# Kernel tuning notes

Hardware: AMD Instinct MI355X
Metric: run time of the kernel (lower is better)

The kernel has to match this reference:

```python
import jax, jax.numpy as jnp
import numpy as np

B, T = 1, 1024
HIDDEN = 5376
N_HEADS = 32
N_KV = 4
HEAD_DIM = 512          # global_head_dim (full-attention layer)
ROT_DIM = 128           # head_dim * full_partial_rotary_factor (0.25)
MAX_SEQ = 4096
THETA = 1000000.0       # full_rope_theta
EPS = 1e-6


def _precompute_freqs(rot_dim, max_seq, theta, freq_base_dim):
    # freq exponent uses full head_dim (freq_base_dim) for partial rotary
    freqs = 1.0 / (theta ** (np.arange(0, rot_dim, 2, dtype=np.float32) / freq_base_dim))
    t = np.arange(max_seq, dtype=np.float32)
    ang = np.outer(t, freqs)                      # [max_seq, rot_dim//2]
    return jnp.asarray(np.cos(ang)), jnp.asarray(np.sin(ang))


def setup_inputs() -> dict:
    key = jax.random.key(0)
    ks = jax.random.split(key, 6)
    x = jax.random.normal(ks[0], (B, T, HIDDEN), jnp.float32)
    wq = jax.random.normal(ks[1], (HIDDEN, N_HEADS * HEAD_DIM), jnp.float32) * 0.02
    wk = jax.random.normal(ks[2], (HIDDEN, N_KV * HEAD_DIM), jnp.float32) * 0.02
    wo = jax.random.normal(ks[3], (N_HEADS * HEAD_DIM, HIDDEN), jnp.float32) * 0.02
    q_norm_w = 1.0 + 0.01 * jax.random.normal(ks[4], (HEAD_DIM,), jnp.float32)
    k_norm_w = 1.0 + 0.01 * jax.random.normal(ks[5], (HEAD_DIM,), jnp.float32)
    input_pos = jnp.arange(T, dtype=jnp.int32)    # prefill positions 0..T-1
    # causal mask over the full cache length: key slot s visible iff s <= query pos
    attn_mask = (jnp.arange(MAX_SEQ)[None, :] <= input_pos[:, None])[None, None]  # [1,1,T,S] bool
    fc, fs = _precompute_freqs(ROT_DIM, MAX_SEQ, THETA, HEAD_DIM)
    k_cache = jnp.zeros((B, N_KV, MAX_SEQ, HEAD_DIM), jnp.float32)
    v_cache = jnp.zeros_like(k_cache)
    return dict(x=x, input_pos=input_pos, attn_mask=attn_mask, wq=wq, wk=wk, wo=wo,
                q_norm_w=q_norm_w, k_norm_w=k_norm_w, k_cache=k_cache, v_cache=v_cache,
                freqs_cos=fc, freqs_sin=fs)


def _rmsnorm(x, w=None):
    y = x * jax.lax.rsqrt(jnp.mean(x * x, axis=-1, keepdims=True) + EPS)
    return y * w if w is not None else y


def _rope(t, cos, sin):
    # t: (B,H,T,D); rotate only the first ROT_DIM dims (interleaved pairs), pass the rest
    rot, pas = t[..., :ROT_DIM], t[..., ROT_DIM:]
    r = rot.reshape(rot.shape[:-1] + (ROT_DIM // 2, 2))
    tr, ti = r[..., 0], r[..., 1]
    c = cos[None, None]  # (1,1,T,ROT_DIM//2)
    s = sin[None, None]
    out = jnp.stack([tr * c - ti * s, tr * s + ti * c], axis=-1).reshape(rot.shape)
    return jnp.concatenate([out, pas], axis=-1)


def reference(x, input_pos, attn_mask, wq, wk, wo, q_norm_w, k_norm_w,
              k_cache, v_cache, freqs_cos, freqs_sin):
    q = (x @ wq).reshape(B, T, N_HEADS, HEAD_DIM)
    raw_k = (x @ wk).reshape(B, T, N_KV, HEAD_DIM)   # k_eq_v: raw_v = raw_k
    q = _rmsnorm(q, q_norm_w)
    k = _rmsnorm(raw_k, k_norm_w)
    v = _rmsnorm(raw_k)                               # RMSNormNoWeight on shared K=V
    q = q.transpose(0, 2, 1, 3)                       # (B,H,T,D)
    k = k.transpose(0, 2, 1, 3)
    v = v.transpose(0, 2, 1, 3)
    cos = freqs_cos[input_pos]
    sin = freqs_sin[input_pos]
    q = _rope(q, cos, sin)
    k = _rope(k, cos, sin)
    # KV cache update (index_copy along seq dim)
    k_cache = k_cache.at[:, :, input_pos, :].set(k)
    v_cache = v_cache.at[:, :, input_pos, :].set(v)
    # GQA SDPA with scale=1.0, grouped to avoid materializing repeated K/V
    G = N_HEADS // N_KV
    qg = q.reshape(B, N_KV, G, T, HEAD_DIM)
    scores = jnp.einsum('bkgtd,bksd->bkgts', qg, k_cache)
    neg = jnp.finfo(scores.dtype).min
    scores = jnp.where(attn_mask[:, :, None], scores, neg)  # (1,1,1,T,S) broadcast
    attn = jax.nn.softmax(scores, axis=-1)
    y = jnp.einsum('bkgts,bksd->bkgtd', attn, v_cache).reshape(B, N_HEADS, T, HEAD_DIM)
    y = y.transpose(0, 2, 1, 3).reshape(B, T, N_HEADS * HEAD_DIM)
    return y @ wo
```

## Files before the change

kernel.cpp:

```cpp
#include <hip/hip_runtime.h>
#include <stdint.h>

typedef unsigned short u16;
typedef _Float16 f16;
typedef f16 f16x8 __attribute__((ext_vector_type(8)));
typedef float f32x4 __attribute__((ext_vector_type(4)));
typedef unsigned short u16x4 __attribute__((ext_vector_type(4)));
typedef unsigned short u16x8 __attribute__((ext_vector_type(8)));

#define MFMA16(a, b, c) __builtin_amdgcn_mfma_f32_16x16x32_f16(a, b, c, 0, 0, 0)

__device__ __forceinline__ u16 f2h_u(float f) {
  union { f16 h; u16 u; } v; v.h = (f16)f; return v.u;
}
__device__ __forceinline__ float h2f(u16 u) {
  union { u16 u; f16 h; } v; v.u = u; return (float)v.h;
}
__device__ __forceinline__ f16x8 ld_h8(const u16* p) {
  return *(const f16x8*)p;
}
__device__ __forceinline__ void gl_lds16(const u16* g, u16* l) {
  __builtin_amdgcn_global_load_lds(
      (const __attribute__((address_space(1))) void*)g,
      (__attribute__((address_space(3))) void*)l, 16, 0, 0);
}

__global__ __launch_bounds__(256) void convert_f32_f16(
    const float* __restrict__ in, u16* __restrict__ out, int n8)
{
  int i = blockIdx.x * 256 + threadIdx.x;
  int stride = gridDim.x * 256;
  for (; i < n8; i += stride) {
    f32x4 a = *(const f32x4*)(in + (size_t)i * 8);
    f32x4 b = *(const f32x4*)(in + (size_t)i * 8 + 4);
    u16x8 o;
#pragma unroll
    for (int j = 0; j < 4; ++j) { o[j] = f2h_u(a[j]); o[4 + j] = f2h_u(b[j]); }
    *(u16x8*)(out + (size_t)i * 8) = o;
  }
}

__global__ __launch_bounds__(256) void transpose_f32_f16(
    const float* __restrict__ in, u16* __restrict__ out,
    int R, int C, int ldi, int ldo)
{
  __shared__ u16 tile[64 * 66];
  int x0 = blockIdx.x * 64, y0 = blockIdx.y * 64;
  int t = threadIdx.x;
  int xr = (t & 15) * 4;
  int yr = t >> 4;
#pragma unroll
  for (int p = 0; p < 4; ++p) {
    int y = yr + p * 16;
    f32x4 v = *(const f32x4*)(in + (size_t)(y0 + y) * ldi + x0 + xr);
    tile[y * 66 + xr + 0] = f2h_u(v[0]);
    tile[y * 66 + xr + 1] = f2h_u(v[1]);
    tile[y * 66 + xr + 2] = f2h_u(v[2]);
    tile[y * 66 + xr + 3] = f2h_u(v[3]);
  }
  __syncthreads();
#pragma unroll
  for (int p = 0; p < 4; ++p) {
    int x = (t >> 4) + p * 16;
    int yq = (t & 15) * 4;
    u16x4 v;
    v.x = tile[(yq + 0) * 66 + x];
    v.y = tile[(yq + 1) * 66 + x];
    v.z = tile[(yq + 2) * 66 + x];
    v.w = tile[(yq + 3) * 66 + x];
    *(u16x4*)(out + (size_t)(x0 + x) * ldo + y0 + yq) = v;
  }
}

__global__ __launch_bounds__(256) void transpose_h16(
    const u16* __restrict__ in, u16* __restrict__ out,
    int R, int C, int ldi, int ldo, long zin, long zout)
{
  __shared__ u16 tile[64 * 66];
  const u16* ip = in + (size_t)blockIdx.z * zin;
  u16* op = out + (size_t)blockIdx.z * zout;
  int x0 = blockIdx.x * 64, y0 = blockIdx.y * 64;
  int t = threadIdx.x;
  int xr = (t & 15) * 4;
  int yr = t >> 4;
#pragma unroll
  for (int p = 0; p < 4; ++p) {
    int y = yr + p * 16;
    u16x4 v = *(const u16x4*)(ip + (size_t)(y0 + y) * ldi + x0 + xr);
    tile[y * 66 + xr + 0] = v.x;
    tile[y * 66 + xr + 1] = v.y;
    tile[y * 66 + xr + 2] = v.z;
    tile[y * 66 + xr + 3] = v.w;
  }
  __syncthreads();
#pragma unroll
  for (int p = 0; p < 4; ++p) {
    int x = (t >> 4) + p * 16;
    int yq = (t & 15) * 4;
    u16x4 v;
    v.x = tile[(yq + 0) * 66 + x];
    v.y = tile[(yq + 1) * 66 + x];
    v.z = tile[(yq + 2) * 66 + x];
    v.w = tile[(yq + 3) * 66 + x];
    *(u16x4*)(op + (size_t)(x0 + x) * ldo + y0 + yq) = v;
  }
}

template <bool F32OUT>
__global__ __launch_bounds__(512, 4) void gemm_bt(
    const u16* __restrict__ A, const u16* __restrict__ Bt, void* __restrict__ Cv,
    int Ksp, int lda, int ldb, int ldc, long zstride)
{
  __shared__ alignas(16) u16 As[3 * 256 * 32];
  __shared__ alignas(16) u16 Bs[3 * 128 * 32];
  int tid = threadIdx.x;
  int lane = tid & 63;
  int wave = tid >> 6;
  int wm = wave >> 2, wn = wave & 3;
  int r15 = lane & 15, g = lane >> 4;

  int gx = gridDim.x, gy = gridDim.y;
  int nwg = gx * gy;
  int flat = blockIdx.y * gx + blockIdx.x;
  int q = nwg >> 3, rr = nwg & 7, xcd = flat & 7, lo = flat >> 3;
  int s = ((xcd < rr) ? xcd * (q + 1) : rr * (q + 1) + (xcd - rr) * q) + lo;
  int by = s % gy;
  int bx = s / gy;
  int row0 = by * 256, col0 = bx * 128;
  int kbeg = blockIdx.z * Ksp;

  int rA = tid >> 2;
  int pc = tid & 3;
  int cs = pc ^ ((rA >> 1) & 3);
  const u16* Ag0 = A  + (size_t)(row0 + rA) * lda + kbeg + cs * 8;
  const u16* Ag1 = Ag0 + (size_t)128 * lda;
  const u16* Bg  = Bt + (size_t)(col0 + rA) * ldb + kbeg + cs * 8;

  f32x4 acc[8][2];
#pragma unroll
  for (int i = 0; i < 8; ++i)
#pragma unroll
    for (int j = 0; j < 2; ++j) acc[i][j] = (f32x4){0.f, 0.f, 0.f, 0.f};

  int nk = Ksp >> 5;

  auto STAGE = [&](int kk, int b) {
    u16* la = As + b * 8192 + wave * 512;
    u16* lb = Bs + b * 4096 + wave * 512;
    gl_lds16(Ag0 + (size_t)kk * 32, la);
    gl_lds16(Ag1 + (size_t)kk * 32, la + 4096);
    gl_lds16(Bg  + (size_t)kk * 32, lb);
  };

  STAGE(0, 0);
  STAGE(1, 1);
  asm volatile("s_waitcnt vmcnt(3)" ::: "memory");
  __builtin_amdgcn_s_barrier();

  int swz = (g ^ ((r15 >> 1) & 3)) * 8;
  int b0 = 0;
  for (int k = 0; k < nk; ++k) {
    const u16* Ab = As + b0 * 8192;
    const u16* Bb = Bs + b0 * 4096;
    f16x8 bfr[2], af[4];
#pragma unroll
    for (int ni = 0; ni < 2; ++ni)
      bfr[ni] = ld_h8(Bb + (wn * 32 + ni * 16 + r15) * 32 + swz);
#pragma unroll
    for (int m2 = 0; m2 < 4; ++m2)
      af[m2] = ld_h8(Ab + (wm * 128 + m2 * 16 + r15) * 32 + swz);
    if (k + 2 < nk) {
      int b2 = b0 + 2; if (b2 >= 3) b2 -= 3;
      STAGE(k + 2, b2);
    }
    __builtin_amdgcn_s_setprio(1);
#pragma unroll
    for (int m2 = 0; m2 < 4; ++m2)
#pragma unroll
      for (int ni = 0; ni < 2; ++ni)
        acc[m2][ni] = MFMA16(af[m2], bfr[ni], acc[m2][ni]);
    f16x8 ag[4];
#pragma unroll
    for (int m2 = 0; m2 < 4; ++m2)
      ag[m2] = ld_h8(Ab + (wm * 128 + (4 + m2) * 16 + r15) * 32 + swz);
#pragma unroll
    for (int m2 = 0; m2 < 4; ++m2)
#pragma unroll
      for (int ni = 0; ni < 2; ++ni)
        acc[4 + m2][ni] = MFMA16(ag[m2], bfr[ni], acc[4 + m2][ni]);
    __builtin_amdgcn_s_setprio(0);
    if (k <= nk - 3) {
      asm volatile("s_waitcnt vmcnt(3)" ::: "memory");
    } else {
      asm volatile("s_waitcnt vmcnt(0)" ::: "memory");
    }
    asm volatile("s_waitcnt lgkmcnt(0)" ::: "memory");
    __builtin_amdgcn_s_barrier();
    b0 = (b0 == 2) ? 0 : b0 + 1;
  }

#pragma unroll
  for (int mi = 0; mi < 8; ++mi)
#pragma unroll
    for (int ni = 0; ni < 2; ++ni) {
      int row = row0 + wm * 128 + mi * 16 + g * 4;
      int col = col0 + wn * 32 + ni * 16 + r15;
#pragma unroll
      for (int r = 0; r < 4; ++r) {
        if constexpr (F32OUT)
          ((float*)Cv)[(size_t)blockIdx.z * zstride + (size_t)(row + r) * ldc + col] = acc[mi][ni][r];
        else
          ((u16*)Cv)[(size_t)(row + r) * ldc + col] = f2h_u(acc[mi][ni][r]);
      }
    }
}

__global__ __launch_bounds__(256) void reduce_add2_f32(
    const float* __restrict__ p, float* __restrict__ out, int n4, long half)
{
  int i = blockIdx.x * 256 + threadIdx.x;
  int stride = gridDim.x * 256;
  for (; i < n4; i += stride) {
    f32x4 a = *(const f32x4*)(p + (size_t)i * 4);
    f32x4 b = *(const f32x4*)(p + half + (size_t)i * 4);
    *(f32x4*)(out + (size_t)i * 4) = a + b;
  }
}

__global__ __launch_bounds__(256) void reduce_add4_f16(
    const float* __restrict__ p, u16* __restrict__ out, int n4, long zs)
{
  int i = blockIdx.x * 256 + threadIdx.x;
  int stride = gridDim.x * 256;
  for (; i < n4; i += stride) {
    f32x4 a = *(const f32x4*)(p + (size_t)i * 4);
    a += *(const f32x4*)(p + zs + (size_t)i * 4);
    a += *(const f32x4*)(p + 2 * zs + (size_t)i * 4);
    a += *(const f32x4*)(p + 3 * zs + (size_t)i * 4);
    u16x4 o;
#pragma unroll
    for (int j = 0; j < 4; ++j) o[j] = f2h_u(a[j]);
    *(u16x4*)(out + (size_t)i * 4) = o;
  }
}

__global__ __launch_bounds__(64) void norm_rope_q(
    u16* __restrict__ q, const float* __restrict__ w,
    const float* __restrict__ fc, const float* __restrict__ fs)
{
  int t = blockIdx.x, h = blockIdx.y, lane = threadIdx.x;
  u16* row = q + (size_t)t * 16384 + h * 512;
  u16x8 v = *(const u16x8*)(row + lane * 8);
  float x[8];
  float ss = 0.f;
#pragma unroll
  for (int j = 0; j < 8; ++j) { x[j] = h2f(v[j]); ss += x[j] * x[j]; }
#pragma unroll
  for (int m = 1; m < 64; m <<= 1) ss += __shfl_xor(ss, m, 64);
  float rms = rsqrtf(ss * (1.f / 512.f) + 1e-6f);
  f32x4 w0 = *(const f32x4*)(w + lane * 8);
  f32x4 w1 = *(const f32x4*)(w + lane * 8 + 4);
  float y[8];
#pragma unroll
  for (int j = 0; j < 4; ++j) {
    y[j] = x[j] * rms * w0[j];
    y[4 + j] = x[4 + j] * rms * w1[j];
  }
  if (lane < 16) {
    f32x4 cv = *(const f32x4*)(fc + t * 64 + lane * 4);
    f32x4 sv = *(const f32x4*)(fs + t * 64 + lane * 4);
#pragma unroll
    for (int j = 0; j < 4; ++j) {
      float c = cv[j], s = sv[j];
      float a = y[2 * j], b = y[2 * j + 1];
      y[2 * j] = a * c - b * s;
      y[2 * j + 1] = a * s + b * c;
    }
  }
  u16x8 o;
#pragma unroll
  for (int j = 0; j < 8; ++j) o[j] = f2h_u(y[j]);
  *(u16x8*)(row + lane * 8) = o;
}

__global__ __launch_bounds__(64) void norm_kv(
    u16* __restrict__ kraw, u16* __restrict__ vout, const float* __restrict__ kw,
    const float* __restrict__ fc, const float* __restrict__ fs)
{
  int t = blockIdx.x, kv = blockIdx.y, lane = threadIdx.x;
  u16* row  = kraw + (size_t)t * 2048 + kv * 512;
  u16* vrow = vout + (size_t)t * 2048 + kv * 512;
  u16x8 v = *(const u16x8*)(row + lane * 8);
  float x[8];
  float ss = 0.f;
#pragma unroll
  for (int j = 0; j < 8; ++j) { x[j] = h2f(v[j]); ss += x[j] * x[j]; }
#pragma unroll
  for (int m = 1; m < 64; m <<= 1) ss += __shfl_xor(ss, m, 64);
  float rms = rsqrtf(ss * (1.f / 512.f) + 1e-6f);
  f32x4 w0 = *(const f32x4*)(kw + lane * 8);
  f32x4 w1 = *(const f32x4*)(kw + lane * 8 + 4);
  float yk[8], yv[8];
#pragma unroll
  for (int j = 0; j < 4; ++j) {
    yv[j] = x[j] * rms;           yv[4 + j] = x[4 + j] * rms;
    yk[j] = yv[j] * w0[j];        yk[4 + j] = yv[4 + j] * w1[j];
  }
  if (lane < 16) {
    f32x4 cv = *(const f32x4*)(fc + t * 64 + lane * 4);
    f32x4 sv = *(const f32x4*)(fs + t * 64 + lane * 4);
#pragma unroll
    for (int j = 0; j < 4; ++j) {
      float c = cv[j], s = sv[j];
      float a = yk[2 * j], b = yk[2 * j + 1];
      yk[2 * j] = a * c - b * s;
      yk[2 * j + 1] = a * s + b * c;
    }
  }
  u16x8 ok, ov;
#pragma unroll
  for (int j = 0; j < 8; ++j) { ok[j] = f2h_u(yk[j]); ov[j] = f2h_u(yv[j]); }
  *(u16x8*)(row + lane * 8) = ok;
  *(u16x8*)(vrow + lane * 8) = ov;
}

__global__ __launch_bounds__(256) void attn2_kernel(
    const u16* __restrict__ Q, const u16* __restrict__ Kb,
    const u16* __restrict__ Vt, u16* __restrict__ Y)
{
  __shared__ float Sred[4 * 32 * 68];
  __shared__ u16 Plds[32 * 64];
  __shared__ float scf[32];
  __shared__ float linv[32];
  __shared__ int nf[4];

  int h = blockIdx.x;
  int qtb = 31 - blockIdx.y;
  int kv = h >> 3;
  int tid = threadIdx.x;
  int lane = tid & 63;
  int w = tid >> 6;
  int r15 = lane & 15, g = lane >> 4;
  int qbase = qtb * 32;
  int dbase = w * 128;

  int jloc = lane >> 3, cl = lane & 7;
  int jrow = w * 8 + jloc;
  int qr_sm = qbase + jrow;

  f16x8 qf[2][4];
  {
    const u16* qp = Q + (size_t)(qbase + r15) * 16384 + h * 512 + dbase + g * 8;
#pragma unroll
    for (int mi = 0; mi < 2; ++mi)
#pragma unroll
      for (int ks = 0; ks < 4; ++ks)
        qf[mi][ks] = ld_h8(qp + (size_t)mi * 16 * 16384 + ks * 32);
  }

  f32x4 acc[2][8];
#pragma unroll
  for (int mi = 0; mi < 2; ++mi)
#pragma unroll
    for (int nt = 0; nt < 8; ++nt) acc[mi][nt] = (f32x4){0.f, 0.f, 0.f, 0.f};
  float m_ = -1e30f, l_ = 0.f;

  const u16* kp_base = Kb + kv * 512 + dbase;
  const u16* vt_base = Vt + (size_t)kv * (512 * 1024) + (size_t)dbase * 1024;
  int nst = (qbase + 31) / 64 + 1;

  for (int st = 0; st < nst; ++st) {
    int s0 = st * 64;
    f32x4 sa[2][4];
#pragma unroll
    for (int mi = 0; mi < 2; ++mi)
#pragma unroll
      for (int nt = 0; nt < 4; ++nt) sa[mi][nt] = (f32x4){0.f, 0.f, 0.f, 0.f};
#pragma unroll
    for (int ks = 0; ks < 4; ++ks) {
#pragma unroll
      for (int nt = 0; nt < 4; ++nt) {
        f16x8 kf = ld_h8(kp_base + (size_t)(s0 + nt * 16 + r15) * 2048 + ks * 32 + g * 8);
#pragma unroll
        for (int mi = 0; mi < 2; ++mi)
          sa[mi][nt] = MFMA16(qf[mi][ks], kf, sa[mi][nt]);
      }
    }
    {
      float* sw = Sred + w * 32 * 68;
#pragma unroll
      for (int mi = 0; mi < 2; ++mi)
#pragma unroll
        for (int nt = 0; nt < 4; ++nt)
#pragma unroll
          for (int r = 0; r < 4; ++r)
            sw[(mi * 16 + g * 4 + r) * 68 + nt * 16 + r15] = sa[mi][nt][r];
    }
    __syncthreads();

    {
      const float* sp = Sred + jrow * 68 + cl * 8;
      f32x4 a0 = *(const f32x4*)(sp);
      f32x4 a1 = *(const f32x4*)(sp + 4);
#pragma unroll
      for (int p = 1; p < 4; ++p) {
        a0 += *(const f32x4*)(sp + p * 32 * 68);
        a1 += *(const f32x4*)(sp + p * 32 * 68 + 4);
      }
      float sv[8];
      int sbase = s0 + cl * 8;
#pragma unroll
      for (int j = 0; j < 4; ++j) {
        sv[j]     = (sbase + j     <= qr_sm) ? a0[j] : -1e30f;
        sv[4 + j] = (sbase + 4 + j <= qr_sm) ? a1[j] : -1e30f;
      }
      float mm = sv[0];
#pragma unroll
      for (int j = 1; j < 8; ++j) mm = fmaxf(mm, sv[j]);
      mm = fmaxf(mm, __shfl_xor(mm, 1, 64));
      mm = fmaxf(mm, __shfl_xor(mm, 2, 64));
      mm = fmaxf(mm, __shfl_xor(mm, 4, 64));
      bool defer = (mm <= m_ + 8.f);
      float sc;
      if (defer) { sc = 1.f; }
      else { float mn = fmaxf(m_, mm); sc = __expf(m_ - mn); m_ = mn; }
      float pv8[8], rsum = 0.f;
#pragma unroll
      for (int j = 0; j < 8; ++j) { pv8[j] = __expf(sv[j] - m_); rsum += pv8[j]; }
      rsum += __shfl_xor(rsum, 1, 64);
      rsum += __shfl_xor(rsum, 2, 64);
      rsum += __shfl_xor(rsum, 4, 64);
      l_ = l_ * sc + rsum;
      u16x8 pw;
#pragma unroll
      for (int j = 0; j < 8; ++j) pw[j] = f2h_u(pv8[j]);
      *(u16x8*)(Plds + jrow * 64 + ((cl ^ (jrow & 7)) * 8)) = pw;
      if (cl == 0) scf[jrow] = sc;
      int need = __any((int)(!defer));
      if (lane == 0) nf[w] = need;
    }
    __syncthreads();

    if (nf[0] | nf[1] | nf[2] | nf[3]) {
#pragma unroll
      for (int mi = 0; mi < 2; ++mi)
#pragma unroll
        for (int r = 0; r < 4; ++r) {
          float s = scf[mi * 16 + g * 4 + r];
#pragma unroll
          for (int nt = 0; nt < 8; ++nt) acc[mi][nt][r] *= s;
        }
    }
    f16x8 pa[2][2];
#pragma unroll
    for (int mi = 0; mi < 2; ++mi)
#pragma unroll
      for (int ks = 0; ks < 2; ++ks) {
        int row = mi * 16 + r15;
        int c = ks * 4 + g;
        pa[mi][ks] = ld_h8(Plds + row * 64 + ((c ^ (row & 7)) * 8));
      }
#pragma unroll
    for (int ks = 0; ks < 2; ++ks)
#pragma unroll
      for (int nt = 0; nt < 8; ++nt) {
        f16x8 vf = ld_h8(vt_base + (size_t)(nt * 16 + r15) * 1024 + s0 + ks * 32 + g * 8);
#pragma unroll
        for (int mi = 0; mi < 2; ++mi)
          acc[mi][nt] = MFMA16(pa[mi][ks], vf, acc[mi][nt]);
      }
  }

  if (cl == 0) linv[jrow] = 1.0f / l_;
  __syncthreads();
#pragma unroll
  for (int mi = 0; mi < 2; ++mi)
#pragma unroll
    for (int r = 0; r < 4; ++r) {
      int row = mi * 16 + g * 4 + r;
      float li = linv[row];
      u16* yp = Y + (size_t)(qbase + row) * 16384 + h * 512 + dbase + r15;
#pragma unroll
      for (int nt = 0; nt < 8; ++nt)
        yp[nt * 16] = f2h_u(acc[mi][nt][r] * li);
    }
}

static inline int imin_h(int a, int b) { return a < b ? a : b; }

extern "C" void kernel_launch(void* const* d_in, const int* in_sizes, int n_in,
                              void* d_out, int out_size, void* d_ws, size_t ws_size,
                              hipStream_t stream)
{
  const float* x  = (const float*)d_in[0];
  const float* wq = (const float*)d_in[3];
  const float* wk = (const float*)d_in[4];
  const float* wo = (const float*)d_in[5];
  const float* qw = (const float*)d_in[6];
  const float* kw = (const float*)d_in[7];
  const float* fc = (const float*)d_in[10];
  const float* fs = (const float*)d_in[11];
  float* out = (float*)d_out;
  char* ws = (char*)d_ws;

  u16* Qbuf = (u16*)(ws + 0);
  u16* Kbuf = (u16*)(ws + 33554432);
  u16* Vbuf = (u16*)(ws + 37748736);
  u16* Vt   = (u16*)(ws + 41943040);
  u16* Ybuf = (u16*)(ws + 46137344);
  u16* xh   = (u16*)(ws + 79691776);
  char* WTb = ws + 91226112;
  size_t cap = (ws_size > 91226112) ? ws_size - 91226112 : 0;
  float* Pb  = (float*)ws;
  float* PbK = (float*)(ws + 46137344);

  convert_f32_f16<<<672, 256, 0, stream>>>(x, xh, (1024 * 5376) / 8);

  {
    const int N = 16384, K = 5376;
    size_t maxNcL = cap / ((size_t)K * 2);
    int Nc = (maxNcL >= (size_t)N) ? N : (int)((maxNcL / 128) * 128);
    if (Nc > 0) {
      u16* WT = (u16*)WTb;
      for (int n0 = 0; n0 < N; n0 += Nc) {
        int nn = imin_h(Nc, N - n0);
        transpose_f32_f16<<<dim3(nn / 64, K / 64), 256, 0, stream>>>(
            wq + n0, WT, K, nn, N, K);
        gemm_bt<false><<<dim3(nn / 128, 4, 1), 512, 0, stream>>>(
            xh, WT, (void*)(Qbuf + n0), K, K, K, 16384, 0L);
      }
    }
  }

  {
    const int N = 2048, K = 5376, Ksp = 1344;
    const long ZS = 2097152L;
    size_t maxNcL = cap / ((size_t)K * 2);
    int Nc = (maxNcL >= (size_t)N) ? N : (int)((maxNcL / 128) * 128);
    if (Nc > 0) {
      u16* WT = (u16*)WTb;
      for (int n0 = 0; n0 < N; n0 += Nc) {
        int nn = imin_h(Nc, N - n0);
        transpose_f32_f16<<<dim3(nn / 64, K / 64), 256, 0, stream>>>(
            wk + n0, WT, K, nn, N, K);
        gemm_bt<true><<<dim3(nn / 128, 4, 4), 512, 0, stream>>>(
            xh, WT, (void*)(PbK + n0), Ksp, K, K, N, ZS);
      }
      reduce_add4_f16<<<2048, 256, 0, stream>>>(PbK, Kbuf, 524288, ZS);
    }
  }

  norm_rope_q<<<dim3(1024, 32), 64, 0, stream>>>(Qbuf, qw, fc, fs);
  norm_kv<<<dim3(1024, 4), 64, 0, stream>>>(Kbuf, Vbuf, kw, fc, fs);
  transpose_h16<<<dim3(8, 16, 4), 256, 0, stream>>>(
      Vbuf, Vt, 1024, 512, 2048, 1024, 512L, 524288L);
  attn2_kernel<<<dim3(32, 32), 256, 0, stream>>>(Qbuf, Kbuf, Vt, Ybuf);

  {
    const int N = 5376, K = 16384, Ksp = 8192;
    const long ZS = 5505024L;
    size_t maxNcL = cap / ((size_t)K * 2);
    int Nc = (maxNcL >= (size_t)N) ? N : (int)((maxNcL / 128) * 128);
    if (Nc > 0) {
      u16* WT = (u16*)WTb;
      for (int n0 = 0; n0 < N; n0 += Nc) {
        int nn = imin_h(Nc, N - n0);
        transpose_f32_f16<<<dim3(nn / 64, K / 64), 256, 0, stream>>>(
            wo + n0, WT, K, nn, N, K);
        gemm_bt<true><<<dim3(nn / 128, 4, 2), 512, 0, stream>>>(
            Ybuf, WT, (void*)(Pb + n0), Ksp, K, K, N, ZS);
      }
      reduce_add2_f32<<<2048, 256, 0, stream>>>(Pb, out, 1376256, ZS);
    }
  }
}
```

Before: 904.9 us.

## Fuse weight fp32-to-fp16 conversion and transpose into GEMM B-tile loading

The separate transpose_f32_f16 passes over wq, wk and wo are removed. Each GEMM now reads fp32 weights directly in K-by-N layout, converts them to fp16 in registers, and writes swizzled tiles into LDS, with one stage of register prefetch alongside the async A loads. This drops a full read-write pass over roughly 200M weight elements and the scratch workspace it needed. In exchange the B path no longer uses direct-to-LDS loads, each thread does eight strided scalar fp32 loads per k-step, and there is extra register pressure and conversion work inside the main loop.

New measurement: 853.5 us. 1.06x faster.

```diff
diff --git a/kernel.cpp b/kernel.cpp
--- a/kernel.cpp
+++ b/kernel.cpp
@@ -37,38 +37,6 @@
 #pragma unroll
     for (int j = 0; j < 4; ++j) { o[j] = f2h_u(a[j]); o[4 + j] = f2h_u(b[j]); }
     *(u16x8*)(out + (size_t)i * 8) = o;
-  }
-}
-
-__global__ __launch_bounds__(256) void transpose_f32_f16(
-    const float* __restrict__ in, u16* __restrict__ out,
-    int R, int C, int ldi, int ldo)
-{
-  __shared__ u16 tile[64 * 66];
-  int x0 = blockIdx.x * 64, y0 = blockIdx.y * 64;
-  int t = threadIdx.x;
-  int xr = (t & 15) * 4;
-  int yr = t >> 4;
-#pragma unroll
-  for (int p = 0; p < 4; ++p) {
-    int y = yr + p * 16;
-    f32x4 v = *(const f32x4*)(in + (size_t)(y0 + y) * ldi + x0 + xr);
-    tile[y * 66 + xr + 0] = f2h_u(v[0]);
-    tile[y * 66 + xr + 1] = f2h_u(v[1]);
-    tile[y * 66 + xr + 2] = f2h_u(v[2]);
-    tile[y * 66 + xr + 3] = f2h_u(v[3]);
-  }
-  __syncthreads();
-#pragma unroll
-  for (int p = 0; p < 4; ++p) {
-    int x = (t >> 4) + p * 16;
-    int yq = (t & 15) * 4;
-    u16x4 v;
-    v.x = tile[(yq + 0) * 66 + x];
-    v.y = tile[(yq + 1) * 66 + x];
-    v.z = tile[(yq + 2) * 66 + x];
-    v.w = tile[(yq + 3) * 66 + x];
-    *(u16x4*)(out + (size_t)(x0 + x) * ldo + y0 + yq) = v;
   }
 }
 
@@ -107,9 +75,9 @@
 }
 
 template <bool F32OUT>
-__global__ __launch_bounds__(512, 4) void gemm_bt(
-    const u16* __restrict__ A, const u16* __restrict__ Bt, void* __restrict__ Cv,
-    int Ksp, int lda, int ldb, int ldc, long zstride)
+__global__ __launch_bounds__(512, 4) void gemm_ktn(
+    const u16* __restrict__ A, const float* __restrict__ W, void* __restrict__ Cv,
+    int Ksp, int lda, int ldw, int ldc, long zstride)
 {
   __shared__ alignas(16) u16 As[3 * 256 * 32];
   __shared__ alignas(16) u16 Bs[3 * 128 * 32];
@@ -132,9 +100,13 @@
   int rA = tid >> 2;
   int pc = tid & 3;
   int cs = pc ^ ((rA >> 1) & 3);
-  const u16* Ag0 = A  + (size_t)(row0 + rA) * lda + kbeg + cs * 8;
+  const u16* Ag0 = A + (size_t)(row0 + rA) * lda + kbeg + cs * 8;
   const u16* Ag1 = Ag0 + (size_t)128 * lda;
-  const u16* Bg  = Bt + (size_t)(col0 + rA) * ldb + kbeg + cs * 8;
+
+  int cB = tid & 127;
+  int kc = tid >> 7;
+  const float* Wg = W + (size_t)(kbeg + kc * 8) * ldw + col0 + cB;
+  int bwoff = cB * 32 + ((kc ^ ((cB >> 1) & 3)) * 8);
 
   f32x4 acc[8][2];
 #pragma unroll
@@ -143,18 +115,31 @@
     for (int j = 0; j < 2; ++j) acc[i][j] = (f32x4){0.f, 0.f, 0.f, 0.f};
 
   int nk = Ksp >> 5;
-
-  auto STAGE = [&](int kk, int b) {
+  float bw[8];
+
+  auto BLOAD = [&](int kk) {
+#pragma unroll
+    for (int j = 0; j < 8; ++j)
+      bw[j] = Wg[(size_t)(kk * 32 + j) * ldw];
+  };
+  auto BWRITE = [&](int b) {
+    u16x8 o;
+#pragma unroll
+    for (int j = 0; j < 8; ++j) o[j] = f2h_u(bw[j]);
+    *(u16x8*)(Bs + b * 4096 + bwoff) = o;
+  };
+  auto STAGE_A = [&](int kk, int b) {
     u16* la = As + b * 8192 + wave * 512;
-    u16* lb = Bs + b * 4096 + wave * 512;
     gl_lds16(Ag0 + (size_t)kk * 32, la);
     gl_lds16(Ag1 + (size_t)kk * 32, la + 4096);
-    gl_lds16(Bg  + (size_t)kk * 32, lb);
   };
 
-  STAGE(0, 0);
-  STAGE(1, 1);
-  asm volatile("s_waitcnt vmcnt(3)" ::: "memory");
+  BLOAD(0);
+  STAGE_A(0, 0);
+  STAGE_A(1, 1);
+  asm volatile("s_waitcnt vmcnt(2)" ::: "memory");
+  BWRITE(0);
+  asm volatile("s_waitcnt lgkmcnt(0)" ::: "memory");
   __builtin_amdgcn_s_barrier();
 
   int swz = (g ^ ((r15 >> 1) & 3)) * 8;
@@ -162,6 +147,11 @@
   for (int k = 0; k < nk; ++k) {
     const u16* Ab = As + b0 * 8192;
     const u16* Bb = Bs + b0 * 4096;
+    if (k + 1 < nk) BLOAD(k + 1);
+    if (k + 2 < nk) {
+      int b2 = b0 + 2; if (b2 >= 3) b2 -= 3;
+      STAGE_A(k + 2, b2);
+    }
     f16x8 bfr[2], af[4];
 #pragma unroll
     for (int ni = 0; ni < 2; ++ni)
@@ -169,10 +159,6 @@
 #pragma unroll
     for (int m2 = 0; m2 < 4; ++m2)
       af[m2] = ld_h8(Ab + (wm * 128 + m2 * 16 + r15) * 32 + swz);
-    if (k + 2 < nk) {
-      int b2 = b0 + 2; if (b2 >= 3) b2 -= 3;
-      STAGE(k + 2, b2);
-    }
     __builtin_amdgcn_s_setprio(1);
 #pragma unroll
     for (int m2 = 0; m2 < 4; ++m2)
@@ -189,10 +175,14 @@
       for (int ni = 0; ni < 2; ++ni)
         acc[4 + m2][ni] = MFMA16(ag[m2], bfr[ni], acc[4 + m2][ni]);
     __builtin_amdgcn_s_setprio(0);
-    if (k <= nk - 3) {
-      asm volatile("s_waitcnt vmcnt(3)" ::: "memory");
-    } else {
-      asm volatile("s_waitcnt vmcnt(0)" ::: "memory");
+    if (k + 1 < nk) {
+      if (k + 2 < nk) {
+        asm volatile("s_waitcnt vmcnt(2)" ::: "memory");
+      } else {
+        asm volatile("s_waitcnt vmcnt(0)" ::: "memory");
+      }
+      int b1 = b0 + 1; if (b1 >= 3) b1 -= 3;
+      BWRITE(b1);
     }
     asm volatile("s_waitcnt lgkmcnt(0)" ::: "memory");
     __builtin_amdgcn_s_barrier();
@@ -210,7 +200,7 @@
         if constexpr (F32OUT)
           ((float*)Cv)[(size_t)blockIdx.z * zstride + (size_t)(row + r) * ldc + col] = acc[mi][ni][r];
         else
-          ((u16*)Cv)[(size_t)(row + r) * ldc + col] = f2h_u(acc[mi][ni][r]);
+          ((u16*)Cv)[(size_t)blockIdx.z * zstride + (size_t)(row + r) * ldc + col] = f2h_u(acc[mi][ni][r]);
       }
     }
 }
@@ -485,8 +475,6 @@
         yp[nt * 16] = f2h_u(acc[mi][nt][r] * li);
     }
 }
-
-static inline int imin_h(int a, int b) { return a < b ? a : b; }
 
 extern "C" void kernel_launch(void* const* d_in, const int* in_sizes, int n_in,
                               void* d_out, int out_size, void* d_ws, size_t ws_size,
@@ -509,46 +497,17 @@
   u16* Vt   = (u16*)(ws + 41943040);
   u16* Ybuf = (u16*)(ws + 46137344);
   u16* xh   = (u16*)(ws + 79691776);
-  char* WTb = ws + 91226112;
-  size_t cap = (ws_size > 91226112) ? ws_size - 91226112 : 0;
   float* Pb  = (float*)ws;
   float* PbK = (float*)(ws + 46137344);
 
   convert_f32_f16<<<672, 256, 0, stream>>>(x, xh, (1024 * 5376) / 8);
 
-  {
-    const int N = 16384, K = 5376;
-    size_t maxNcL = cap / ((size_t)K * 2);
-    int Nc = (maxNcL >= (size_t)N) ? N : (int)((maxNcL / 128) * 128);
-    if (Nc > 0) {
-      u16* WT = (u16*)WTb;
-      for (int n0 = 0; n0 < N; n0 += Nc) {
-        int nn = imin_h(Nc, N - n0);
-        transpose_f32_f16<<<dim3(nn / 64, K / 64), 256, 0, stream>>>(
-            wq + n0, WT, K, nn, N, K);
-        gemm_bt<false><<<dim3(nn / 128, 4, 1), 512, 0, stream>>>(
-            xh, WT, (void*)(Qbuf + n0), K, K, K, 16384, 0L);
-      }
-    }
-  }
-
-  {
-    const int N = 2048, K = 5376, Ksp = 1344;
-    const long ZS = 2097152L;
-    size_t maxNcL = cap / ((size_t)K * 2);
-    int Nc = (maxNcL >= (size_t)N) ? N : (int)((maxNcL / 128) * 128);
-    if (Nc > 0) {
-      u16* WT = (u16*)WTb;
-      for (int n0 = 0; n0 < N; n0 += Nc) {
-        int nn = imin_h(Nc, N - n0);
-        transpose_f32_f16<<<dim3(nn / 64, K / 64), 256, 0, stream>>>(
-            wk + n0, WT, K, nn, N, K);
-        gemm_bt<true><<<dim3(nn / 128, 4, 4), 512, 0, stream>>>(
-            xh, WT, (void*)(PbK + n0), Ksp, K, K, N, ZS);
-      }
-      reduce_add4_f16<<<2048, 256, 0, stream>>>(PbK, Kbuf, 524288, ZS);
-    }
-  }
+  gemm_ktn<false><<<dim3(128, 4, 1), 512, 0, stream>>>(
+      xh, wq, (void*)Qbuf, 5376, 5376, 16384, 16384, 0L);
+
+  gemm_ktn<true><<<dim3(16, 4, 4), 512, 0, stream>>>(
+      xh, wk, (void*)PbK, 1344, 5376, 2048, 2048, 2097152L);
+  reduce_add4_f16<<<2048, 256, 0, stream>>>(PbK, Kbuf, 524288, 2097152L);
 
   norm_rope_q<<<dim3(1024, 32), 64, 0, stream>>>(Qbuf, qw, fc, fs);
   norm_kv<<<dim3(1024, 4), 64, 0, stream>>>(Kbuf, Vbuf, kw, fc, fs);
@@ -556,21 +515,7 @@
       Vbuf, Vt, 1024, 512, 2048, 1024, 512L, 524288L);
   attn2_kernel<<<dim3(32, 32), 256, 0, stream>>>(Qbuf, Kbuf, Vt, Ybuf);
 
-  {
-    const int N = 5376, K = 16384, Ksp = 8192;
-    const long ZS = 5505024L;
-    size_t maxNcL = cap / ((size_t)K * 2);
-    int Nc = (maxNcL >= (size_t)N) ? N : (int)((maxNcL / 128) * 128);
-    if (Nc > 0) {
-      u16* WT = (u16*)WTb;
-      for (int n0 = 0; n0 < N; n0 += Nc) {
-        int nn = imin_h(Nc, N - n0);
-        transpose_f32_f16<<<dim3(nn / 64, K / 64), 256, 0, stream>>>(
-            wo + n0, WT, K, nn, N, K);
-        gemm_bt<true><<<dim3(nn / 128, 4, 2), 512, 0, stream>>>(
-            Ybuf, WT, (void*)(Pb + n0), Ksp, K, K, N, ZS);
-      }
-      reduce_add2_f32<<<2048, 256, 0, stream>>>(Pb, out, 1376256, ZS);
-    }
-  }
-}
+  gemm_ktn<true><<<dim3(42, 4, 2), 512, 0, stream>>>(
+      Ybuf, wo, (void*)Pb, 8192, 16384, 5376, 5376, 5505024L);
+  reduce_add2_f32<<<2048, 256, 0, stream>>>(Pb, out, 1376256, 5505024L);
+}
```
